# Optimization experiments

Hardware: AMD Instinct MI355X
Metric: run time of the kernel (lower is better)

The kernel has to match this reference:

```python
import jax, jax.numpy as jnp
import numpy as np

H, C = 8, 32          # heads, out_channels per head (H*C = 256)
D = H * C
NEG_SLOPE = 0.2
SELF_LOOP_TYPE = 6    # num_edge_types - 1
EPS_LN = 1e-5
EPS_BN = 1e-5


def _gat_layer(x, src, dst, ea, et, Ws, Wd, a_s, a_d, We, ae, te, Wo, bo, b, lg, lb):
    N = x.shape[0]
    xs = (x @ Ws).reshape(N, H, C)   # lin_src -> x_j features
    xd = (x @ Wd).reshape(N, H, C)   # lin_dst -> x_i features
    # per-node attention logits (gathered per edge): alpha = <x_i, att_src> + <x_j, att_dst>
    a_i = jnp.einsum('nhc,hc->nh', xd, a_s)  # paired with x_i (dst)
    a_j = jnp.einsum('nhc,hc->nh', xs, a_d)  # paired with x_j (src)
    alpha = a_i[dst] + a_j[src]                                  # [E, H]
    ef = (ea @ We).reshape(-1, H, C)                              # lin_edge
    alpha = alpha + jnp.einsum('ehc,hc->eh', ef, ae)
    tf = te[et].reshape(-1, H, C)                                 # edge_type_emb
    alpha = alpha + jnp.einsum('ehc,hc->eh', tf, ae)
    alpha = jnp.where(alpha >= 0, alpha, NEG_SLOPE * alpha)       # leaky_relu
    # segment softmax over destination nodes (every node has a self loop)
    m = jax.ops.segment_max(alpha, dst, num_segments=N)
    e = jnp.exp(alpha - m[dst])
    s = jax.ops.segment_sum(e, dst, num_segments=N)
    alpha = e / (s[dst] + 1e-16)                                  # [E, H]
    # dropout is identity in eval mode
    msg = xs[src] * alpha[:, :, None]                             # [E, H, C]
    out = jax.ops.segment_sum(msg, dst, num_segments=N).reshape(N, D)
    out = out @ Wo + bo + b                                       # lin_out + bias
    mu = out.mean(-1, keepdims=True)
    var = out.var(-1, keepdims=True)
    out = (out - mu) / jnp.sqrt(var + EPS_LN) * lg + lb           # layer norm
    return out + x                                                # in_channels == H*C residual


def _bn_relu(x, g, bvec, relu=True):
    mu = x.mean(0)
    var = x.var(0)
    x = (x - mu) / jnp.sqrt(var + EPS_BN) * g + bvec
    return jnp.maximum(x, 0.0) if relu else x


def _forward(x, edge_index, edge_attr, edge_types,
             Ws1, Wd1, as1, ad1, We1, ae1, te1, Wo1, bo1, b1, lg1, lb1,
             Ws2, Wd2, as2, ad2, We2, ae2, te2, Wo2, bo2, b2, lg2, lb2,
             bng1, bnb1, bng2, bnb2):
    N = x.shape[0]
    loops = jnp.arange(N, dtype=edge_index.dtype)
    src = jnp.concatenate([edge_index[0], loops])
    dst = jnp.concatenate([edge_index[1], loops])
    ea = jnp.concatenate([edge_attr, jnp.ones((N, edge_attr.shape[1]), edge_attr.dtype)])
    et = jnp.concatenate([edge_types, jnp.full((N,), SELF_LOOP_TYPE, edge_types.dtype)])
    residual = x  # in_channels == out_channels -> identity projection
    out = _gat_layer(x, src, dst, ea, et, Ws1, Wd1, as1, ad1, We1, ae1, te1, Wo1, bo1, b1, lg1, lb1)
    out = _bn_relu(out, bng1, bnb1, relu=True)   # dropout identity in eval
    out = _gat_layer(out, src, dst, ea, et, Ws2, Wd2, as2, ad2, We2, ae2, te2, Wo2, bo2, b2, lg2, lb2)
    out = _bn_relu(out, bng2, bnb2, relu=False)
    return jnp.maximum(out + residual, 0.0)


def setup_inputs() -> dict:
    key = jax.random.key(0)
    ks = jax.random.split(key, 32)
    N, E, EDIM, NTYPES = 20000, 320000, 16, 7
    d = {}
    d['x'] = jax.random.normal(ks[0], (N, D), jnp.float32)
    d['edge_index'] = jax.random.randint(ks[1], (2, E), 0, N, jnp.int64)
    d['edge_attr'] = jax.random.normal(ks[2], (E, EDIM), jnp.float32)
    d['edge_types'] = jax.random.randint(ks[3], (E,), 0, NTYPES, jnp.int64)
    def glorot(k, shape):
        fan = shape[-2] + shape[-1] if len(shape) >= 2 else shape[-1] + 1
        return jax.random.uniform(k, shape, jnp.float32, -1.0, 1.0) * np.sqrt(6.0 / fan)
    i = 4
    for L in ('1', '2'):
        d['Ws' + L] = glorot(ks[i], (D, D)); i += 1
        d['Wd' + L] = glorot(ks[i], (D, D)); i += 1
        d['as' + L] = glorot(ks[i], (H, C)); i += 1
        d['ad' + L] = glorot(ks[i], (H, C)); i += 1
        d['We' + L] = glorot(ks[i], (EDIM, D)); i += 1
        d['ae' + L] = glorot(ks[i], (H, C)); i += 1
        d['te' + L] = glorot(ks[i], (NTYPES, D)); i += 1
        d['Wo' + L] = glorot(ks[i], (D, D)); i += 1
        d['bo' + L] = jnp.zeros((D,), jnp.float32)
        d['b' + L] = jnp.zeros((D,), jnp.float32)
        d['lg' + L] = jnp.ones((D,), jnp.float32)
        d['lb' + L] = jnp.zeros((D,), jnp.float32)
    d['bng1'] = jnp.ones((D,), jnp.float32); d['bnb1'] = jnp.zeros((D,), jnp.float32)
    d['bng2'] = jnp.ones((D,), jnp.float32); d['bnb2'] = jnp.zeros((D,), jnp.float32)
    return d


def reference(x, edge_index, edge_attr, edge_types,
              Ws1, Wd1, as1, ad1, We1, ae1, te1, Wo1, bo1, b1, lg1, lb1,
              Ws2, Wd2, as2, ad2, We2, ae2, te2, Wo2, bo2, b2, lg2, lb2,
              bng1, bnb1, bng2, bnb2):
    return _forward(x, edge_index, edge_attr, edge_types,
                    Ws1, Wd1, as1, ad1, We1, ae1, te1, Wo1, bo1, b1, lg1, lb1,
                    Ws2, Wd2, as2, ad2, We2, ae2, te2, Wo2, bo2, b2, lg2, lb2,
                    bng1, bnb1, bng2, bnb2)
```

## Files before the change

kernel.cpp:

```cpp
#include <hip/hip_runtime.h>

#define DD 256
#define HH 8
#define CC 32

typedef __attribute__((ext_vector_type(8))) short short8;
typedef __attribute__((ext_vector_type(4))) float f32x4;

static __device__ __forceinline__ unsigned short f2b(float f){
  unsigned u = __float_as_uint(f);
  u = u + 0x7FFFu + ((u >> 16) & 1u);
  return (unsigned short)(u >> 16);
}
static __device__ __forceinline__ float b2f(unsigned short s){
  return __uint_as_float(((unsigned)s) << 16);
}

static __device__ __forceinline__ void gload16(const void* g, void* l){
  using gpt = const __attribute__((address_space(1))) unsigned int*;
  using lpt = __attribute__((address_space(3))) unsigned int*;
  __builtin_amdgcn_global_load_lds((gpt)(unsigned long long)g, (lpt)(unsigned long long)l, 16, 0, 0);
}

__global__ void k_zero_i(int* p, int n){ int i=blockIdx.x*blockDim.x+threadIdx.x; if(i<n) p[i]=0; }

__global__ void k_count(const int* __restrict__ dstE, int E, int N, int* cnt){
  int e=blockIdx.x*blockDim.x+threadIdx.x;
  if(e<E+N){ int d=(e<E)? dstE[e] : (e-E); atomicAdd(&cnt[d],1); }
}

__global__ __launch_bounds__(1024) void k_scan(const int* __restrict__ cnt, int N, int* row_off, int* cursor){
  __shared__ int part[1024];
  int t=threadIdx.x;
  int chunk=(N+1023)>>10;
  int s=0;
  for(int j=0;j<chunk;j++){ int i=t*chunk+j; if(i<N) s+=cnt[i]; }
  part[t]=s; __syncthreads();
  for(int off=1; off<1024; off<<=1){
    int v=(t>=off)? part[t-off]:0;
    __syncthreads();
    part[t]+=v;
    __syncthreads();
  }
  int run=(t==0)?0:part[t-1];
  for(int j=0;j<chunk;j++){ int i=t*chunk+j; if(i<N){ row_off[i]=run; cursor[i]=run; run+=cnt[i]; } }
  if(t==1023) row_off[N]=part[1023];
}

__global__ void k_fill(const int* __restrict__ srcE, const int* __restrict__ dstE,
                       const float* __restrict__ ea, const int* __restrict__ et,
                       int E, int N, int* cursor,
                       int* esrc, int* etP, float* eaP){
  int e=blockIdx.x*blockDim.x+threadIdx.x;
  if(e>=E+N) return;
  int s,d,ty;
  float4 q0,q1,q2,q3;
  if(e<E){
    s=srcE[e]; d=dstE[e]; ty=et[e];
    q0=*(const float4*)&ea[(size_t)e*16+0];
    q1=*(const float4*)&ea[(size_t)e*16+4];
    q2=*(const float4*)&ea[(size_t)e*16+8];
    q3=*(const float4*)&ea[(size_t)e*16+12];
  }else{
    s=e-E; d=s; ty=6;
    q0=q1=q2=q3=make_float4(1.f,1.f,1.f,1.f);
  }
  int pos=atomicAdd(&cursor[d],1);
  esrc[pos]=s; etP[pos]=ty;
  float* o=&eaP[(size_t)pos*16];
  *(float4*)(o+0)=q0; *(float4*)(o+4)=q1; *(float4*)(o+8)=q2; *(float4*)(o+12)=q3;
}

__global__ void k_cvt_wT4(const float* __restrict__ W0, const float* __restrict__ W1,
                          const float* __restrict__ W2, const float* __restrict__ W3,
                          unsigned short* __restrict__ T0, unsigned short* __restrict__ T1,
                          unsigned short* __restrict__ T2, unsigned short* __restrict__ T3){
  int m=blockIdx.y, c=blockIdx.x, k=threadIdx.x;
  const float* W = (m==0)?W0:(m==1)?W1:(m==2)?W2:W3;
  unsigned short* T = (m==0)?T0:(m==1)?T1:(m==2)?T2:T3;
  T[(size_t)c*DD+k] = f2b(W[(size_t)k*DD+c]);
}

__global__ void k_pre2(const float* __restrict__ Wd1, const float* __restrict__ as1,
                       const float* __restrict__ We1, const float* __restrict__ ae1,
                       const float* __restrict__ te1,
                       const float* __restrict__ Wd2, const float* __restrict__ as2,
                       const float* __restrict__ We2, const float* __restrict__ ae2,
                       const float* __restrict__ te2,
                       float* wd_as1, float* v_e1, float* t_a1,
                       float* wd_as2, float* v_e2, float* t_a2){
  int L=blockIdx.x;
  const float* Wd=L?Wd2:Wd1; const float* as_=L?as2:as1;
  const float* We=L?We2:We1; const float* ae=L?ae2:ae1; const float* te=L?te2:te1;
  float* wd_as=L?wd_as2:wd_as1; float* v_e=L?v_e2:v_e1; float* t_a=L?t_a2:t_a1;
  int t=threadIdx.x;
  for(int idx=t; idx<DD*HH; idx+=256){
    int k=idx>>3, h=idx&7;
    const float* w=&Wd[k*DD+h*CC]; const float* a=&as_[h*CC];
    float s=0;
    #pragma unroll
    for(int c=0;c<CC;c++) s+=w[c]*a[c];
    wd_as[idx]=s;
  }
  for(int idx=t; idx<16*HH; idx+=256){
    int k=idx>>3, h=idx&7;
    const float* w=&We[k*DD+h*CC]; const float* a=&ae[h*CC];
    float s=0;
    #pragma unroll
    for(int c=0;c<CC;c++) s+=w[c]*a[c];
    v_e[idx]=s;
  }
  for(int idx=t; idx<7*HH; idx+=256){
    int k=idx>>3, h=idx&7;
    const float* w=&te[k*DD+h*CC]; const float* a=&ae[h*CC];
    float s=0;
    #pragma unroll
    for(int c=0;c<CC;c++) s+=w[c]*a[c];
    t_a[idx]=s;
  }
}

#define NB_BA 1024
__global__ __launch_bounds__(256) void k_cvt_x2(const float* __restrict__ xin, const float* __restrict__ wd_as,
                         unsigned short* __restrict__ xb, float* __restrict__ a_i, int N){
  int b=blockIdx.x, tid=threadIdx.x, wv=tid>>6, l=tid&63;
  int c0=4*l;
  float wa[4][8];
  #pragma unroll
  for(int j=0;j<4;j++)
    #pragma unroll
    for(int h=0;h<8;h++) wa[j][h]=wd_as[(c0+j)*8+h];
  for(int n=b*4+wv; n<N; n+=NB_BA*4){
    float4 v=*(const float4*)&xin[(size_t)n*DD+c0];
    ushort4 xo; xo.x=f2b(v.x); xo.y=f2b(v.y); xo.z=f2b(v.z); xo.w=f2b(v.w);
    *(ushort4*)&xb[(size_t)n*DD+c0]=xo;
    float ai[8];
    #pragma unroll
    for(int h=0;h<8;h++) ai[h]=v.x*wa[0][h]+v.y*wa[1][h]+v.z*wa[2][h]+v.w*wa[3][h];
    #pragma unroll
    for(int off=1;off<64;off<<=1){
      #pragma unroll
      for(int h=0;h<8;h++) ai[h]+=__shfl_xor(ai[h],off);
    }
    if(l==0){
      float4 A; A.x=ai[0];A.y=ai[1];A.z=ai[2];A.w=ai[3];
      float4 B; B.x=ai[4];B.y=ai[5];B.z=ai[6];B.w=ai[7];
      *(float4*)&a_i[(size_t)n*HH]=A;
      *(float4*)&a_i[(size_t)n*HH+4]=B;
    }
  }
}

template<bool AJ>
__global__ __launch_bounds__(256) void k_gemm1(const unsigned short* __restrict__ A,
                                               const unsigned short* __restrict__ Bt,
                                               const float* __restrict__ ad, float* __restrict__ a_j,
                                               unsigned short* __restrict__ Cout, int N){
  __shared__ char lds[2*12288];
  int tid=threadIdx.x;
  int w=tid>>6, l=tid&63;
  int row0=blockIdx.y*64, col0=blockIdx.x*128;

  int lr=l>>2;
  int kc=(l&3)^((l>>3)&3);
  const unsigned short* ga  = &A [(size_t)(row0+16*w+lr)*DD + kc*8];
  const unsigned short* gb0 = &Bt[(size_t)(col0+32*w+lr)*DD + kc*8];
  const unsigned short* gb1 = &Bt[(size_t)(col0+32*w+16+lr)*DD + kc*8];
  int laoff =      w*1024;
  int lboff0=4096+(32*w)*64;
  int lboff1=4096+(32*w+16)*64;

  int x15=l&15;
  int lp=x15*64 + ((l>>4)^((x15>>1)&3))*16;

  f32x4 acc[4][2];
  #pragma unroll
  for(int i=0;i<4;i++){ acc[i][0]=(f32x4)0.f; acc[i][1]=(f32x4)0.f; }

  gload16(ga,  lds+laoff);
  gload16(gb0, lds+lboff0);
  gload16(gb1, lds+lboff1);
  __syncthreads();
  int cur=0;
  for(int kt=0;kt<DD;kt+=32){
    int nxt=cur^1;
    if(kt+32<DD){
      gload16(ga +kt+32, lds+nxt*12288+laoff);
      gload16(gb0+kt+32, lds+nxt*12288+lboff0);
      gload16(gb1+kt+32, lds+nxt*12288+lboff1);
    }
    char* base=lds+cur*12288;
    short8 af[4], bf[2];
    #pragma unroll
    for(int mf=0;mf<4;mf++) af[mf]=*(short8*)(base + mf*1024 + lp);
    #pragma unroll
    for(int nf=0;nf<2;nf++) bf[nf]=*(short8*)(base + 4096 + (32*w+16*nf)*64 + lp);
    #pragma unroll
    for(int mf=0;mf<4;mf++)
      #pragma unroll
      for(int nf=0;nf<2;nf++)
        acc[mf][nf]=__builtin_amdgcn_mfma_f32_16x16x32_bf16(af[mf],bf[nf],acc[mf][nf],0,0,0);
    __syncthreads();
    cur=nxt;
  }

  int lcol=x15, lrow4=(l>>4)*4;
  float ad0=0.f, ad1=0.f;
  if(AJ){ ad0=ad[col0+32*w+lcol]; ad1=ad[col0+32*w+16+lcol]; }
  int head=(col0>>5)+w;
  #pragma unroll
  for(int mf=0;mf<4;mf++){
    #pragma unroll
    for(int nf=0;nf<2;nf++){
      int col=col0 + 32*w + 16*nf + lcol;
      #pragma unroll
      for(int rr=0;rr<4;rr++){
        int row=row0 + 16*mf + lrow4 + rr;
        if(row<N) Cout[(size_t)row*DD+col]=f2b(acc[mf][nf][rr]);
      }
    }
    if(AJ){
      #pragma unroll
      for(int rr=0;rr<4;rr++){
        float t=acc[mf][0][rr]*ad0 + acc[mf][1][rr]*ad1;
        t+=__shfl_xor(t,1); t+=__shfl_xor(t,2);
        t+=__shfl_xor(t,4); t+=__shfl_xor(t,8);
        int row=row0 + 16*mf + lrow4 + rr;
        if(x15==0 && row<N) a_j[(size_t)row*HH+head]=t;
      }
    }
  }
}

__global__ __launch_bounds__(256) void k_gemm_ln(const unsigned short* __restrict__ A,
                                                 const unsigned short* __restrict__ Bt,
                                                 const float* __restrict__ bo, const float* __restrict__ bvec,
                                                 const float* __restrict__ xin,
                                                 const float* __restrict__ lg, const float* __restrict__ lb,
                                                 float* __restrict__ hout,
                                                 float* __restrict__ psum, float* __restrict__ psq, int N){
  __shared__ char lds[2*18432];
  int tid=threadIdx.x;
  int w=tid>>6, l=tid&63;
  int row0=blockIdx.x*32;

  int lr=l>>2;
  int kc=(l&3)^((l>>3)&3);
  const unsigned short* ga = &A[(size_t)(row0+16*w+lr)*DD + kc*8];
  const unsigned short* gb0=&Bt[(size_t)(64*w   +lr)*DD + kc*8];
  const unsigned short* gb1=&Bt[(size_t)(64*w+16+lr)*DD + kc*8];
  const unsigned short* gb2=&Bt[(size_t)(64*w+32+lr)*DD + kc*8];
  const unsigned short* gb3=&Bt[(size_t)(64*w+48+lr)*DD + kc*8];
  int laoff =      w*1024;
  int lboff0=2048+(64*w   )*64;
  int lboff1=2048+(64*w+16)*64;
  int lboff2=2048+(64*w+32)*64;
  int lboff3=2048+(64*w+48)*64;

  int x15=l&15;
  int lp=x15*64 + ((l>>4)^((x15>>1)&3))*16;

  f32x4 acc[2][4];
  #pragma unroll
  for(int i=0;i<2;i++)
    #pragma unroll
    for(int j=0;j<4;j++) acc[i][j]=(f32x4)0.f;

  if(w<2) gload16(ga, lds+laoff);
  gload16(gb0, lds+lboff0);
  gload16(gb1, lds+lboff1);
  gload16(gb2, lds+lboff2);
  gload16(gb3, lds+lboff3);
  __syncthreads();
  int cur=0;
  for(int kt=0;kt<DD;kt+=32){
    int nxt=cur^1;
    if(kt+32<DD){
      char* nb=lds+nxt*18432;
      if(w<2) gload16(ga+kt+32, nb+laoff);
      gload16(gb0+kt+32, nb+lboff0);
      gload16(gb1+kt+32, nb+lboff1);
      gload16(gb2+kt+32, nb+lboff2);
      gload16(gb3+kt+32, nb+lboff3);
    }
    char* base=lds+cur*18432;
    short8 af[2], bf[4];
    #pragma unroll
    for(int mf=0;mf<2;mf++) af[mf]=*(short8*)(base + mf*1024 + lp);
    #pragma unroll
    for(int nf=0;nf<4;nf++) bf[nf]=*(short8*)(base + 2048 + (64*w+16*nf)*64 + lp);
    #pragma unroll
    for(int mf=0;mf<2;mf++)
      #pragma unroll
      for(int nf=0;nf<4;nf++)
        acc[mf][nf]=__builtin_amdgcn_mfma_f32_16x16x32_bf16(af[mf],bf[nf],acc[mf][nf],0,0,0);
    __syncthreads();
    cur=nxt;
  }

  int lrow4=(l>>4)*4;
  float lgv[4], lbv[4];
  #pragma unroll
  for(int nf=0;nf<4;nf++){
    int col=64*w+16*nf+x15;
    float badd=bo[col]+bvec[col];
    lgv[nf]=lg[col]; lbv[nf]=lb[col];
    #pragma unroll
    for(int mf=0;mf<2;mf++)
      #pragma unroll
      for(int rr=0;rr<4;rr++) acc[mf][nf][rr]+=badd;
  }
  __syncthreads();
  float* rs   =(float*)lds;
  float* rq   =(float*)(lds+512);
  float* mus  =(float*)(lds+1024);
  float* rstds=(float*)(lds+1152);
  #pragma unroll
  for(int mf=0;mf<2;mf++){
    #pragma unroll
    for(int rr=0;rr<4;rr++){
      float t=acc[mf][0][rr]+acc[mf][1][rr]+acc[mf][2][rr]+acc[mf][3][rr];
      float q=acc[mf][0][rr]*acc[mf][0][rr]+acc[mf][1][rr]*acc[mf][1][rr]
             +acc[mf][2][rr]*acc[mf][2][rr]+acc[mf][3][rr]*acc[mf][3][rr];
      t+=__shfl_xor(t,1); q+=__shfl_xor(q,1);
      t+=__shfl_xor(t,2); q+=__shfl_xor(q,2);
      t+=__shfl_xor(t,4); q+=__shfl_xor(q,4);
      t+=__shfl_xor(t,8); q+=__shfl_xor(q,8);
      if(x15==0){
        int row=16*mf+lrow4+rr;
        rs[w*32+row]=t; rq[w*32+row]=q;
      }
    }
  }
  __syncthreads();
  if(tid<32){
    float S=rs[tid]+rs[32+tid]+rs[64+tid]+rs[96+tid];
    float Q=rq[tid]+rq[32+tid]+rq[64+tid]+rq[96+tid];
    float mu=S*(1.f/DD);
    float var=Q*(1.f/DD)-mu*mu;
    mus[tid]=mu;
    rstds[tid]=rsqrtf(var+1e-5f);
  }
  __syncthreads();
  float cps[4]={0.f,0.f,0.f,0.f}, cqs[4]={0.f,0.f,0.f,0.f};
  #pragma unroll
  for(int mf=0;mf<2;mf++){
    #pragma unroll
    for(int rr=0;rr<4;rr++){
      int row=16*mf+lrow4+rr;
      int grow=row0+row;
      bool ok=(grow<N);
      float mu=mus[row], rstd=rstds[row];
      #pragma unroll
      for(int nf=0;nf<4;nf++){
        int col=64*w+16*nf+x15;
        float h=0.f;
        if(ok){
          h=(acc[mf][nf][rr]-mu)*rstd*lgv[nf]+lbv[nf]+xin[(size_t)grow*DD+col];
          hout[(size_t)grow*DD+col]=h;
        }
        cps[nf]+=h; cqs[nf]+=h*h;
      }
    }
  }
  #pragma unroll
  for(int nf=0;nf<4;nf++){
    cps[nf]+=__shfl_xor(cps[nf],16); cqs[nf]+=__shfl_xor(cqs[nf],16);
    cps[nf]+=__shfl_xor(cps[nf],32); cqs[nf]+=__shfl_xor(cqs[nf],32);
  }
  if(l<16){
    #pragma unroll
    for(int nf=0;nf<4;nf++){
      int col=64*w+16*nf+l;
      psum[(size_t)blockIdx.x*DD+col]=cps[nf];
      psq [(size_t)blockIdx.x*DD+col]=cqs[nf];
    }
  }
}

__global__ __launch_bounds__(256) void k_agg(const int* __restrict__ row_off,
                      const int* __restrict__ esrc, const int* __restrict__ etP,
                      const float* __restrict__ eaP,
                      const float* __restrict__ a_i, const float* __restrict__ a_j,
                      const float* __restrict__ v_e, const float* __restrict__ t_a,
                      const unsigned short* __restrict__ ysb, unsigned short* __restrict__ aggb, int N){
  int wv=threadIdx.x>>6, l=threadIdx.x&63;
  int n=blockIdx.x*4+wv;
  if(n>=N) return;
  int beg=row_off[n], deg=row_off[n+1]-beg;
  int slotL=l>>3, headL=l&7;
  int half=l>>5, lk=l&31;
  int hh=lk>>2;
  float veh[16];
  #pragma unroll
  for(int k=0;k<16;k++) veh[k]=v_e[k*8+headL];
  float aih=a_i[(size_t)n*HH+headL];
  float m=-3e38f, ssum=0.f;
  float acc[8];
  #pragma unroll
  for(int j=0;j<8;j++) acc[j]=0.f;
  for(int base=0;base<deg;base+=8){
    int i=base+slotL;
    bool ok=(i<deg);
    int ic=ok?i:(deg-1);
    size_t pos=(size_t)(beg+ic);
    int src=esrc[pos];
    float v=-3e38f;
    {
      int ty=etP[pos];
      float aj=a_j[(size_t)src*HH+headL];
      const float* eap=&eaP[pos*16];
      float4 q0=*(const float4*)(eap+0);
      float4 q1=*(const float4*)(eap+4);
      float4 q2=*(const float4*)(eap+8);
      float4 q3=*(const float4*)(eap+12);
      float t=aih+aj+t_a[ty*8+headL];
      t+=q0.x*veh[0]+q0.y*veh[1]+q0.z*veh[2]+q0.w*veh[3];
      t+=q1.x*veh[4]+q1.y*veh[5]+q1.z*veh[6]+q1.w*veh[7];
      t+=q2.x*veh[8]+q2.y*veh[9]+q2.z*veh[10]+q2.w*veh[11];
      t+=q3.x*veh[12]+q3.y*veh[13]+q3.z*veh[14]+q3.w*veh[15];
      t=(t>=0.f)? t : 0.2f*t;
      if(ok) v=t;
    }
    float cm=v;
    cm=fmaxf(cm,__shfl_xor(cm,8));
    cm=fmaxf(cm,__shfl_xor(cm,16));
    cm=fmaxf(cm,__shfl_xor(cm,32));
    float cmg=__shfl(cm,hh);
    float mnew=fmaxf(m,cmg);
    float f=__expf(m-mnew);
    ssum*=f;
    #pragma unroll
    for(int j=0;j<8;j++) acc[j]*=f;
    m=mnew;
    int cnt=min(8,deg-base);
    #pragma unroll
    for(int u=0;u<8;u+=2){
      int e=u+half;
      float vu=__shfl(v,(e<<3)|hh);
      int   si=__shfl(src,(e<<3));
      if(e<cnt){
        float wgt=__expf(vu-m);
        ssum+=wgt;
        short8 y=*(const short8*)&ysb[(size_t)si*DD+8*lk];
        #pragma unroll
        for(int j=0;j<8;j++) acc[j]+=wgt*b2f((unsigned short)y[j]);
      }
    }
  }
  ssum+=__shfl_xor(ssum,32);
  #pragma unroll
  for(int j=0;j<8;j++) acc[j]+=__shfl_xor(acc[j],32);
  if(half==0){
    float inv=1.f/(ssum+1e-16f);
    short8 o;
    #pragma unroll
    for(int j=0;j<8;j++) o[j]=(short)f2b(acc[j]*inv);
    *(short8*)&aggb[(size_t)n*DD+8*lk]=o;
  }
}

__global__ __launch_bounds__(256) void k_bnfin(const float* __restrict__ psum, const float* __restrict__ psq,
                        const float* __restrict__ g, const float* __restrict__ b,
                        float* scale, float* shift, int N, int nb){
  __shared__ float rs[256], rq[256];
  int c=blockIdx.x, tid=threadIdx.x;
  float s=0.f,q=0.f;
  for(int i=tid;i<nb;i+=256){ s+=psum[(size_t)i*DD+c]; q+=psq[(size_t)i*DD+c]; }
  rs[tid]=s; rq[tid]=q;
  __syncthreads();
  #pragma unroll
  for(int off=128;off>0;off>>=1){
    if(tid<off){ rs[tid]+=rs[tid+off]; rq[tid]+=rq[tid+off]; }
    __syncthreads();
  }
  if(tid==0){
    float inv=1.f/(float)N;
    float mu=rs[0]*inv;
    float var=rq[0]*inv - mu*mu;
    float sc=g[c]*rsqrtf(var+1e-5f);
    scale[c]=sc;
    shift[c]=b[c]-mu*sc;
  }
}

template<bool RES, bool CVT>
__global__ __launch_bounds__(256) void k_bnapply(const float* __restrict__ hm, const float* __restrict__ scale,
                          const float* __restrict__ shift, const float* __restrict__ res,
                          float* __restrict__ outp, unsigned short* __restrict__ xb,
                          const float* __restrict__ wd_as, float* __restrict__ a_i, int N){
  int b=blockIdx.x, tid=threadIdx.x, wv=tid>>6, l=tid&63;
  int c0=4*l;
  float4 sc=*(const float4*)&scale[c0];
  float4 sh=*(const float4*)&shift[c0];
  float wa[4][8];
  if(CVT){
    #pragma unroll
    for(int j=0;j<4;j++)
      #pragma unroll
      for(int h=0;h<8;h++) wa[j][h]=wd_as[(c0+j)*8+h];
  }
  for(int n=b*4+wv; n<N; n+=NB_BA*4){
    float4 v=*(const float4*)&hm[(size_t)n*DD+c0];
    v.x=v.x*sc.x+sh.x; v.y=v.y*sc.y+sh.y; v.z=v.z*sc.z+sh.z; v.w=v.w*sc.w+sh.w;
    if(RES){
      float4 rr=*(const float4*)&res[(size_t)n*DD+c0];
      v.x+=rr.x; v.y+=rr.y; v.z+=rr.z; v.w+=rr.w;
    }
    v.x=fmaxf(v.x,0.f); v.y=fmaxf(v.y,0.f); v.z=fmaxf(v.z,0.f); v.w=fmaxf(v.w,0.f);
    *(float4*)&outp[(size_t)n*DD+c0]=v;
    if(CVT){
      ushort4 xo; xo.x=f2b(v.x); xo.y=f2b(v.y); xo.z=f2b(v.z); xo.w=f2b(v.w);
      *(ushort4*)&xb[(size_t)n*DD+c0]=xo;
      float ai[8];
      #pragma unroll
      for(int h=0;h<8;h++) ai[h]=v.x*wa[0][h]+v.y*wa[1][h]+v.z*wa[2][h]+v.w*wa[3][h];
      #pragma unroll
      for(int off=1;off<64;off<<=1){
        #pragma unroll
        for(int h=0;h<8;h++) ai[h]+=__shfl_xor(ai[h],off);
      }
      if(l==0){
        float4 A; A.x=ai[0];A.y=ai[1];A.z=ai[2];A.w=ai[3];
        float4 B; B.x=ai[4];B.y=ai[5];B.z=ai[6];B.w=ai[7];
        *(float4*)&a_i[(size_t)n*HH]=A;
        *(float4*)&a_i[(size_t)n*HH+4]=B;
      }
    }
  }
}

extern "C" void kernel_launch(void* const* d_in, const int* in_sizes, int n_in,
                              void* d_out, int out_size, void* d_ws, size_t ws_size,
                              hipStream_t stream) {
  const float* x  = (const float*)d_in[0];
  const int*   ei = (const int*)d_in[1];
  const float* ea = (const float*)d_in[2];
  const int*   et = (const int*)d_in[3];
  int N = in_sizes[0]/DD;
  int E = in_sizes[3];
  int Etot = E+N;
  const int* srcE = ei;
  const int* dstE = ei + E;

  const float* Ws1=(const float*)d_in[4];  const float* Wd1=(const float*)d_in[5];
  const float* as1=(const float*)d_in[6];  const float* ad1=(const float*)d_in[7];
  const float* We1=(const float*)d_in[8];  const float* ae1=(const float*)d_in[9];
  const float* te1=(const float*)d_in[10]; const float* Wo1=(const float*)d_in[11];
  const float* bo1=(const float*)d_in[12]; const float* b1 =(const float*)d_in[13];
  const float* lg1=(const float*)d_in[14]; const float* lb1=(const float*)d_in[15];
  const float* Ws2=(const float*)d_in[16]; const float* Wd2=(const float*)d_in[17];
  const float* as2=(const float*)d_in[18]; const float* ad2=(const float*)d_in[19];
  const float* We2=(const float*)d_in[20]; const float* ae2=(const float*)d_in[21];
  const float* te2=(const float*)d_in[22]; const float* Wo2=(const float*)d_in[23];
  const float* bo2=(const float*)d_in[24]; const float* b2 =(const float*)d_in[25];
  const float* lg2=(const float*)d_in[26]; const float* lb2=(const float*)d_in[27];
  const float* bng1=(const float*)d_in[28]; const float* bnb1=(const float*)d_in[29];
  const float* bng2=(const float*)d_in[30]; const float* bnb2=(const float*)d_in[31];

  char* p=(char*)d_ws;
  auto alloc=[&](size_t bytes)->void*{ void* r=(void*)p; p+=(bytes+255)&~(size_t)255; return r; };
  unsigned short* xb   =(unsigned short*)alloc((size_t)N*DD*2);
  unsigned short* ysb  =(unsigned short*)alloc((size_t)N*DD*2);
  unsigned short* aggb =(unsigned short*)alloc((size_t)N*DD*2);
  float* eaP   =(float*)alloc((size_t)Etot*16*4);
  int*   etP   =(int*)alloc((size_t)Etot*4);
  float* xout1 =(float*)alloc((size_t)N*DD*4);
  float* a_i   =(float*)alloc((size_t)N*HH*4);
  float* a_j   =(float*)alloc((size_t)N*HH*4);
  float* wd_as1=(float*)alloc(DD*HH*4);
  float* v_e1  =(float*)alloc(16*HH*4);
  float* t_a1  =(float*)alloc(7*HH*4);
  float* wd_as2=(float*)alloc(DD*HH*4);
  float* v_e2  =(float*)alloc(16*HH*4);
  float* t_a2  =(float*)alloc(7*HH*4);
  int nbLN=(N+31)/32;
  float* psum  =(float*)alloc((size_t)nbLN*DD*4);
  float* psq   =(float*)alloc((size_t)nbLN*DD*4);
  float* scl   =(float*)alloc(256*4);
  float* shf   =(float*)alloc(256*4);
  unsigned short* Wsb1T=(unsigned short*)alloc((size_t)DD*DD*2);
  unsigned short* Wob1T=(unsigned short*)alloc((size_t)DD*DD*2);
  unsigned short* Wsb2T=(unsigned short*)alloc((size_t)DD*DD*2);
  unsigned short* Wob2T=(unsigned short*)alloc((size_t)DD*DD*2);
  int* cnt     =(int*)alloc((size_t)N*4);
  int* row_off =(int*)alloc((size_t)(N+1)*4);
  int* cursor  =(int*)alloc((size_t)N*4);
  int* esrc    =(int*)alloc((size_t)Etot*4);
  float* hbuf  =(float*)d_out;

  dim3 gg(2,(N+63)/64);
  int aggGrid=(N+3)/4;

  k_zero_i<<<(N+255)/256,256,0,stream>>>(cnt,N);
  k_count<<<(Etot+255)/256,256,0,stream>>>(dstE,E,N,cnt);
  k_scan<<<1,1024,0,stream>>>(cnt,N,row_off,cursor);
  k_fill<<<(Etot+255)/256,256,0,stream>>>(srcE,dstE,ea,et,E,N,cursor,esrc,etP,eaP);
  k_cvt_wT4<<<dim3(DD,4),DD,0,stream>>>(Ws1,Wo1,Ws2,Wo2,Wsb1T,Wob1T,Wsb2T,Wob2T);
  k_pre2<<<2,256,0,stream>>>(Wd1,as1,We1,ae1,te1,Wd2,as2,We2,ae2,te2,
                             wd_as1,v_e1,t_a1,wd_as2,v_e2,t_a2);

  k_cvt_x2<<<NB_BA,256,0,stream>>>(x,wd_as1,xb,a_i,N);
  k_gemm1<true><<<gg,256,0,stream>>>(xb,Wsb1T,ad1,a_j,ysb,N);
  k_agg<<<aggGrid,256,0,stream>>>(row_off,esrc,etP,eaP,a_i,a_j,v_e1,t_a1,ysb,aggb,N);
  k_gemm_ln<<<nbLN,256,0,stream>>>(aggb,Wob1T,bo1,b1,x,lg1,lb1,hbuf,psum,psq,N);
  k_bnfin<<<DD,256,0,stream>>>(psum,psq,bng1,bnb1,scl,shf,N,nbLN);
  k_bnapply<false,true><<<NB_BA,256,0,stream>>>(hbuf,scl,shf,nullptr,xout1,xb,wd_as2,a_i,N);

  k_gemm1<true><<<gg,256,0,stream>>>(xb,Wsb2T,ad2,a_j,ysb,N);
  k_agg<<<aggGrid,256,0,stream>>>(row_off,esrc,etP,eaP,a_i,a_j,v_e2,t_a2,ysb,aggb,N);
  k_gemm_ln<<<nbLN,256,0,stream>>>(aggb,Wob2T,bo2,b2,xout1,lg2,lb2,hbuf,psum,psq,N);
  k_bnfin<<<DD,256,0,stream>>>(psum,psq,bng2,bnb2,scl,shf,N,nbLN);
  k_bnapply<true,false><<<NB_BA,256,0,stream>>>(hbuf,scl,shf,x,(float*)d_out,nullptr,nullptr,nullptr,N);
}
```

Baseline: 311.4 us.

## Pack edge src/type, store edge attrs as bf16, prefetch next edge batch in aggregation

The CSR fill kernel now packs the source index and edge type into one int and stores the 16 edge attributes as bf16 instead of fp32. This halves edge-attribute traffic and drops one index array. The aggregation kernel software-pipelines its edge loop, loading the next batch's packed index, attributes and a_j before computing the current batch, to hide gather latency. The cost is bf16 rounding of edge attributes in the attention logits and extra registers for the prefetched data.

```diff
diff --git a/kernel.cpp b/kernel.cpp
--- a/kernel.cpp
+++ b/kernel.cpp
@@ -50,25 +50,33 @@
 __global__ void k_fill(const int* __restrict__ srcE, const int* __restrict__ dstE,
                        const float* __restrict__ ea, const int* __restrict__ et,
                        int E, int N, int* cursor,
-                       int* esrc, int* etP, float* eaP){
+                       int* stP, unsigned short* eaPb){
   int e=blockIdx.x*blockDim.x+threadIdx.x;
   if(e>=E+N) return;
   int s,d,ty;
-  float4 q0,q1,q2,q3;
+  float q[16];
   if(e<E){
     s=srcE[e]; d=dstE[e]; ty=et[e];
-    q0=*(const float4*)&ea[(size_t)e*16+0];
-    q1=*(const float4*)&ea[(size_t)e*16+4];
-    q2=*(const float4*)&ea[(size_t)e*16+8];
-    q3=*(const float4*)&ea[(size_t)e*16+12];
+    float4 q0=*(const float4*)&ea[(size_t)e*16+0];
+    float4 q1=*(const float4*)&ea[(size_t)e*16+4];
+    float4 q2=*(const float4*)&ea[(size_t)e*16+8];
+    float4 q3=*(const float4*)&ea[(size_t)e*16+12];
+    q[0]=q0.x;q[1]=q0.y;q[2]=q0.z;q[3]=q0.w;
+    q[4]=q1.x;q[5]=q1.y;q[6]=q1.z;q[7]=q1.w;
+    q[8]=q2.x;q[9]=q2.y;q[10]=q2.z;q[11]=q2.w;
+    q[12]=q3.x;q[13]=q3.y;q[14]=q3.z;q[15]=q3.w;
   }else{
     s=e-E; d=s; ty=6;
-    q0=q1=q2=q3=make_float4(1.f,1.f,1.f,1.f);
+    #pragma unroll
+    for(int j=0;j<16;j++) q[j]=1.f;
   }
   int pos=atomicAdd(&cursor[d],1);
-  esrc[pos]=s; etP[pos]=ty;
-  float* o=&eaP[(size_t)pos*16];
-  *(float4*)(o+0)=q0; *(float4*)(o+4)=q1; *(float4*)(o+8)=q2; *(float4*)(o+12)=q3;
+  stP[pos]= s | (ty<<24);
+  short8 o0,o1;
+  #pragma unroll
+  for(int j=0;j<8;j++){ o0[j]=(short)f2b(q[j]); o1[j]=(short)f2b(q[8+j]); }
+  *(short8*)&eaPb[(size_t)pos*16]=o0;
+  *(short8*)&eaPb[(size_t)pos*16+8]=o1;
 }
 
 __global__ void k_cvt_wT4(const float* __restrict__ W0, const float* __restrict__ W1,
@@ -379,8 +387,7 @@
 }
 
 __global__ __launch_bounds__(256) void k_agg(const int* __restrict__ row_off,
-                      const int* __restrict__ esrc, const int* __restrict__ etP,
-                      const float* __restrict__ eaP,
+                      const int* __restrict__ stP, const unsigned short* __restrict__ eaPb,
                       const float* __restrict__ a_i, const float* __restrict__ a_j,
                       const float* __restrict__ v_e, const float* __restrict__ t_a,
                       const unsigned short* __restrict__ ysb, unsigned short* __restrict__ aggb, int N){
@@ -399,29 +406,32 @@
   float acc[8];
   #pragma unroll
   for(int j=0;j<8;j++) acc[j]=0.f;
+
+  int ic0 = (slotL<deg)? slotL : (deg-1);
+  size_t pos0=(size_t)(beg+ic0);
+  int st_c = stP[pos0];
+  short8 e0_c=*(const short8*)&eaPb[pos0*16];
+  short8 e1_c=*(const short8*)&eaPb[pos0*16+8];
+  float aj_c = a_j[(size_t)(st_c&0xFFFFFF)*HH+headL];
+
   for(int base=0;base<deg;base+=8){
-    int i=base+slotL;
-    bool ok=(i<deg);
-    int ic=ok?i:(deg-1);
-    size_t pos=(size_t)(beg+ic);
-    int src=esrc[pos];
-    float v=-3e38f;
-    {
-      int ty=etP[pos];
-      float aj=a_j[(size_t)src*HH+headL];
-      const float* eap=&eaP[pos*16];
-      float4 q0=*(const float4*)(eap+0);
-      float4 q1=*(const float4*)(eap+4);
-      float4 q2=*(const float4*)(eap+8);
-      float4 q3=*(const float4*)(eap+12);
-      float t=aih+aj+t_a[ty*8+headL];
-      t+=q0.x*veh[0]+q0.y*veh[1]+q0.z*veh[2]+q0.w*veh[3];
-      t+=q1.x*veh[4]+q1.y*veh[5]+q1.z*veh[6]+q1.w*veh[7];
-      t+=q2.x*veh[8]+q2.y*veh[9]+q2.z*veh[10]+q2.w*veh[11];
-      t+=q3.x*veh[12]+q3.y*veh[13]+q3.z*veh[14]+q3.w*veh[15];
-      t=(t>=0.f)? t : 0.2f*t;
-      if(ok) v=t;
-    }
+    bool ok=(base+slotL)<deg;
+    int in_=base+8+slotL;
+    int icn=(in_<deg)? in_ : (deg-1);
+    size_t posn=(size_t)(beg+icn);
+    int st_n = stP[posn];
+    short8 e0_n=*(const short8*)&eaPb[posn*16];
+    short8 e1_n=*(const short8*)&eaPb[posn*16+8];
+    float aj_n = a_j[(size_t)(st_n&0xFFFFFF)*HH+headL];
+    int src = st_c & 0xFFFFFF;
+    int ty  = ((unsigned)st_c) >> 24;
+    float t = aih + aj_c + t_a[ty*8+headL];
+    #pragma unroll
+    for(int j=0;j<8;j++) t += b2f((unsigned short)e0_c[j])*veh[j];
+    #pragma unroll
+    for(int j=0;j<8;j++) t += b2f((unsigned short)e1_c[j])*veh[8+j];
+    t=(t>=0.f)? t : 0.2f*t;
+    float v = ok ? t : -3e38f;
     float cm=v;
     cm=fmaxf(cm,__shfl_xor(cm,8));
     cm=fmaxf(cm,__shfl_xor(cm,16));
@@ -447,6 +457,7 @@
         for(int j=0;j<8;j++) acc[j]+=wgt*b2f((unsigned short)y[j]);
       }
     }
+    st_c=st_n; e0_c=e0_n; e1_c=e1_n; aj_c=aj_n;
   }
   ssum+=__shfl_xor(ssum,32);
   #pragma unroll
@@ -563,8 +574,8 @@
   unsigned short* xb   =(unsigned short*)alloc((size_t)N*DD*2);
   unsigned short* ysb  =(unsigned short*)alloc((size_t)N*DD*2);
   unsigned short* aggb =(unsigned short*)alloc((size_t)N*DD*2);
-  float* eaP   =(float*)alloc((size_t)Etot*16*4);
-  int*   etP   =(int*)alloc((size_t)Etot*4);
+  unsigned short* eaPb =(unsigned short*)alloc((size_t)Etot*16*2);
+  int*   stP   =(int*)alloc((size_t)Etot*4);
   float* xout1 =(float*)alloc((size_t)N*DD*4);
   float* a_i   =(float*)alloc((size_t)N*HH*4);
   float* a_j   =(float*)alloc((size_t)N*HH*4);
@@ -586,7 +597,6 @@
   int* cnt     =(int*)alloc((size_t)N*4);
   int* row_off =(int*)alloc((size_t)(N+1)*4);
   int* cursor  =(int*)alloc((size_t)N*4);
-  int* esrc    =(int*)alloc((size_t)Etot*4);
   float* hbuf  =(float*)d_out;
 
   dim3 gg(2,(N+63)/64);
@@ -595,20 +605,20 @@
   k_zero_i<<<(N+255)/256,256,0,stream>>>(cnt,N);
   k_count<<<(Etot+255)/256,256,0,stream>>>(dstE,E,N,cnt);
   k_scan<<<1,1024,0,stream>>>(cnt,N,row_off,cursor);
-  k_fill<<<(Etot+255)/256,256,0,stream>>>(srcE,dstE,ea,et,E,N,cursor,esrc,etP,eaP);
+  k_fill<<<(Etot+255)/256,256,0,stream>>>(srcE,dstE,ea,et,E,N,cursor,stP,eaPb);
   k_cvt_wT4<<<dim3(DD,4),DD,0,stream>>>(Ws1,Wo1,Ws2,Wo2,Wsb1T,Wob1T,Wsb2T,Wob2T);
   k_pre2<<<2,256,0,stream>>>(Wd1,as1,We1,ae1,te1,Wd2,as2,We2,ae2,te2,
                              wd_as1,v_e1,t_a1,wd_as2,v_e2,t_a2);
 
   k_cvt_x2<<<NB_BA,256,0,stream>>>(x,wd_as1,xb,a_i,N);
   k_gemm1<true><<<gg,256,0,stream>>>(xb,Wsb1T,ad1,a_j,ysb,N);
-  k_agg<<<aggGrid,256,0,stream>>>(row_off,esrc,etP,eaP,a_i,a_j,v_e1,t_a1,ysb,aggb,N);
+  k_agg<<<aggGrid,256,0,stream>>>(row_off,stP,eaPb,a_i,a_j,v_e1,t_a1,ysb,aggb,N);
   k_gemm_ln<<<nbLN,256,0,stream>>>(aggb,Wob1T,bo1,b1,x,lg1,lb1,hbuf,psum,psq,N);
   k_bnfin<<<DD,256,0,stream>>>(psum,psq,bng1,bnb1,scl,shf,N,nbLN);
   k_bnapply<false,true><<<NB_BA,256,0,stream>>>(hbuf,scl,shf,nullptr,xout1,xb,wd_as2,a_i,N);
 
   k_gemm1<true><<<gg,256,0,stream>>>(xb,Wsb2T,ad2,a_j,ysb,N);
-  k_agg<<<aggGrid,256,0,stream>>>(row_off,esrc,etP,eaP,a_i,a_j,v_e2,t_a2,ysb,aggb,N);
+  k_agg<<<aggGrid,256,0,stream>>>(row_off,stP,eaPb,a_i,a_j,v_e2,t_a2,ysb,aggb,N);
   k_gemm_ln<<<nbLN,256,0,stream>>>(aggb,Wob2T,bo2,b2,xout1,lg2,lb2,hbuf,psum,psq,N);
   k_bnfin<<<DD,256,0,stream>>>(psum,psq,bng2,bnb2,scl,shf,N,nbLN);
   k_bnapply<true,false><<<NB_BA,256,0,stream>>>(hbuf,scl,shf,x,(float*)d_out,nullptr,nullptr,nullptr,N);
```

Measured after the change: 297.9 us. 4.3% less time.
